# Performance work log

Measured on AMD Instinct MI355X. Metric: run time of the kernel, lower is better.

## Reference

```python
import jax, jax.numpy as jnp
import numpy as np

V = 12288      # HEALPix vertices (nside=32)
C_IN = 128
C_OUT = 128
K = 4          # Chebyshev polynomial degree
DEG = 9        # nnz per Laplacian row (8 neighbors + self)
B = 8
BN_EPS = 1e-5


def setup_inputs() -> dict:
    key = jax.random.key(0)
    kx, kc, kv, kw = jax.random.split(key, 4)
    x = jax.random.normal(kx, (B, V, C_IN), dtype=jnp.float32)
    # sparse Laplacian as COO edge list: 9 entries per row
    lap_rows = jnp.repeat(jnp.arange(V, dtype=jnp.int32), DEG)          # [E]
    lap_cols = jax.random.randint(kc, (V * DEG,), 0, V, dtype=jnp.int32)
    lap_vals = jax.random.normal(kv, (V * DEG,), dtype=jnp.float32) * 0.1
    # Chebyshev weight [Fin*K, Fout] (Fin-major, K-minor, matching [B,V,Fin,K] reshape)
    weight = jax.random.normal(kw, (C_IN * K, C_OUT), dtype=jnp.float32) * (1.0 / np.sqrt(C_IN * K))
    gamma = jnp.ones((C_OUT,), dtype=jnp.float32)
    beta = jnp.zeros((C_OUT,), dtype=jnp.float32)
    return {"x": x, "lap_rows": lap_rows, "lap_cols": lap_cols,
            "lap_vals": lap_vals, "weight": weight, "gamma": gamma, "beta": beta}


def reference(x, lap_rows, lap_cols, lap_vals, weight, gamma, beta):
    b, v, c = x.shape
    k = weight.shape[0] // c

    def spmm(y):
        # y: [B, V, C] -> L @ y along vertex dim
        y2 = y.transpose(1, 0, 2).reshape(v, b * c)                 # [V, B*C]
        g = lap_vals[:, None] * y2[lap_cols]                        # [E, B*C]
        out = jnp.zeros((v, b * c), dtype=y.dtype).at[lap_rows].add(g)
        return out.reshape(v, b, c).transpose(1, 0, 2)              # [B, V, C]

    # Chebyshev recursion: T0 = x, T1 = L x, Tk = 2 L T_{k-1} - T_{k-2}
    terms = [x]
    if k > 1:
        terms.append(spmm(x))
    for _ in range(2, k):
        terms.append(2.0 * spmm(terms[-1]) - terms[-2])
    xk = jnp.stack(terms, axis=-1)                                  # [B, V, C, K]
    conv = jnp.einsum('bvck,cko->bvo', xk.reshape(b, v, c, k),
                      weight.reshape(c, k, -1))                     # [B, V, Cout]

    # BatchNorm1d over [B, Cout, V]: stats over (batch, vertices) per channel
    h = conv.transpose(0, 2, 1)                                     # [B, Cout, V]
    mean = jnp.mean(h, axis=(0, 2), keepdims=True)
    var = jnp.var(h, axis=(0, 2), keepdims=True)
    hn = (h - mean) * jax.lax.rsqrt(var + BN_EPS)
    return hn * gamma[None, :, None] + beta[None, :, None]          # [B, Cout, V]
```

## Files before the change

### kernel.cpp

```cpp
#include <hip/hip_runtime.h>

#define NV    12288
#define CIN   128
#define COUT  128
#define DEG   9
#define NB    8
#define NROWS (NB * NV)
#define KTOT  512
#define BM    384

typedef unsigned short bfu;
typedef __attribute__((ext_vector_type(8))) short short8;
typedef __attribute__((ext_vector_type(4))) float floatx4;

__device__ __forceinline__ float bf2f(unsigned short u) {
    union { unsigned int i; float f; } x;
    x.i = ((unsigned int)u) << 16;
    return x.f;
}
__device__ __forceinline__ unsigned short f2bf(float f) {
    union { float f; unsigned int i; } x;
    x.f = f;
    unsigned int r = x.i + 0x7FFFu + ((x.i >> 16) & 1u);
    return (unsigned short)(r >> 16);
}
__device__ __forceinline__ void gload16(const void* g, void* l) {
    __builtin_amdgcn_global_load_lds(
        (const __attribute__((address_space(1))) unsigned int*)g,
        (__attribute__((address_space(3))) unsigned int*)l, 16, 0, 0);
}

__global__ __launch_bounds__(256)
void prep_kernel(const float* __restrict__ x, bfu* __restrict__ xb,
                 const float* __restrict__ W, bfu* __restrict__ Wt,
                 float* __restrict__ stats)
{
    const int blk = blockIdx.x;
    const int t   = threadIdx.x;
    if (blk < 6144) {
        const size_t i = ((size_t)blk * 256 + t) * 8;
        const float4 a = *reinterpret_cast<const float4*>(x + i);
        const float4 b = *reinterpret_cast<const float4*>(x + i + 4);
        short8 r;
        r[0] = (short)f2bf(a.x); r[1] = (short)f2bf(a.y);
        r[2] = (short)f2bf(a.z); r[3] = (short)f2bf(a.w);
        r[4] = (short)f2bf(b.x); r[5] = (short)f2bf(b.y);
        r[6] = (short)f2bf(b.z); r[7] = (short)f2bf(b.w);
        *reinterpret_cast<short8*>(xb + i) = r;
    } else if (blk < 6400) {
        const int i = (blk - 6144) * 256 + t;
        const int o = i >> 9;
        const int kap = i & 511;
        const int s = kap >> 7;
        const int c = kap & 127;
        Wt[i] = f2bf(W[(size_t)(c * 4 + s) * COUT + o]);
    } else {
        stats[t] = 0.f;
        if (t == 0) stats[2 * COUT] = 0.f;
    }
}

__global__ __launch_bounds__(256)
void spmm_bf16(const bfu* __restrict__ src, const bfu* __restrict__ sub,
               bfu* __restrict__ outp, const int* __restrict__ cols,
               const float* __restrict__ vals)
{
    const int t  = threadIdx.x;
    const int b  = blockIdx.x & 7;
    const int vt = blockIdx.x >> 3;
    const int v  = vt * 16 + (t >> 4);
    const int c0 = (t & 15) * 8;

    int   ec[DEG];
    float ev[DEG];
#pragma unroll
    for (int e = 0; e < DEG; ++e) {
        ec[e] = cols[v * DEG + e];
        ev[e] = vals[v * DEG + e];
    }

    float acc[8];
#pragma unroll
    for (int j = 0; j < 8; ++j) acc[j] = 0.f;

    const size_t bbase = (size_t)b * NV * CIN;
#pragma unroll
    for (int e = 0; e < DEG; ++e) {
        const short8 s = *reinterpret_cast<const short8*>(
            src + bbase + (size_t)ec[e] * CIN + c0);
#pragma unroll
        for (int j = 0; j < 8; ++j)
            acc[j] = fmaf(ev[e], bf2f((unsigned short)s[j]), acc[j]);
    }

    if (sub != nullptr) {
        const short8 s0 = *reinterpret_cast<const short8*>(
            sub + bbase + (size_t)v * CIN + c0);
#pragma unroll
        for (int j = 0; j < 8; ++j)
            acc[j] = 2.f * acc[j] - bf2f((unsigned short)s0[j]);
    }

    short8 r;
#pragma unroll
    for (int j = 0; j < 8; ++j) r[j] = (short)f2bf(acc[j]);
    *reinterpret_cast<short8*>(outp + bbase + (size_t)v * CIN + c0) = r;
}

__global__ __launch_bounds__(512, 2)
void gemm_mfma(const bfu* __restrict__ A0, const bfu* __restrict__ A1,
               const bfu* __restrict__ A2, const bfu* __restrict__ A3,
               const bfu* __restrict__ Wt, float* __restrict__ gstats,
               const float* __restrict__ gamma, const float* __restrict__ beta,
               float* __restrict__ outp)
{
    extern __shared__ char smem[];

    const int t    = threadIdx.x;
    const int lane = t & 63;
    const int wid  = t >> 6;
    const int wr   = wid >> 1;
    const int wc   = wid & 1;
    const int rbase = blockIdx.x * BM;

    floatx4 acc[6][4];
#pragma unroll
    for (int m = 0; m < 6; ++m)
#pragma unroll
        for (int n = 0; n < 4; ++n) acc[m][n] = (floatx4){0.f, 0.f, 0.f, 0.f};

    const bfu* segs[4] = {A0, A1, A2, A3};

#define STAGE(KT, BUF)                                                        \
    {                                                                         \
        const bfu* As_ = segs[(KT) >> 2];                                     \
        const int  cb_ = ((KT) & 3) * 32;                                     \
        _Pragma("unroll")                                                     \
        for (int p = 0; p < 3; ++p) {                                         \
            const int flat = p * 512 + t;                                     \
            const int rr   = flat >> 2;                                       \
            const int ck   = flat & 3;                                        \
            gload16(As_ + (size_t)(rbase + rr) * CIN + cb_                    \
                        + ((ck ^ ((rr >> 1) & 3)) << 3),                      \
                    smem + (BUF) * 24576 + flat * 16);                        \
        }                                                                     \
        {                                                                     \
            const int nn = t >> 2;                                            \
            const int ck = t & 3;                                             \
            gload16(Wt + (size_t)nn * KTOT + (KT) * 32                        \
                       + ((ck ^ ((nn >> 1) & 3)) << 3),                       \
                    smem + 73728 + (BUF) * 8192 + t * 16);                    \
        }                                                                     \
    }

    STAGE(0, 0);
    STAGE(1, 1);
    asm volatile("s_waitcnt vmcnt(4)\n\ts_barrier" ::: "memory");

    const int rsw   = ((lane & 15) >> 1) & 3;
    const int chunk = ((lane >> 4) ^ rsw) * 16;

#pragma unroll
    for (int kt = 0; kt < 16; ++kt) {
        if (kt + 2 < 16) STAGE(kt + 2, (kt + 2) % 3);

        const char* abase = smem + (kt % 3) * 24576;
        const char* bbase = smem + 73728 + (kt % 3) * 8192;
        short8 a[6], b[4];
#pragma unroll
        for (int m = 0; m < 6; ++m)
            a[m] = *reinterpret_cast<const short8*>(
                abase + (wr * 96 + m * 16 + (lane & 15)) * 64 + chunk);
#pragma unroll
        for (int n = 0; n < 4; ++n)
            b[n] = *reinterpret_cast<const short8*>(
                bbase + (wc * 64 + n * 16 + (lane & 15)) * 64 + chunk);
#pragma unroll
        for (int m = 0; m < 6; ++m)
#pragma unroll
            for (int n = 0; n < 4; ++n)
                acc[m][n] = __builtin_amdgcn_mfma_f32_16x16x32_bf16(
                    a[m], b[n], acc[m][n], 0, 0, 0);

        if (kt <= 13)
            asm volatile("s_waitcnt vmcnt(4)\n\ts_barrier" ::: "memory");
        else if (kt == 14)
            asm volatile("s_waitcnt vmcnt(0)\n\ts_barrier" ::: "memory");
    }
#undef STAGE

    __syncthreads();
    float* sred = (float*)smem;
    float* qred = sred + COUT;
    if (t < COUT) { sred[t] = 0.f; qred[t] = 0.f; }
    __syncthreads();

    const int batch = rbase / NV;
    const int v0 = (rbase % NV) + wr * 96 + (lane >> 4) * 4;
    const int ob = wc * 64 + (lane & 15);

#pragma unroll
    for (int n = 0; n < 4; ++n) {
        const int o = ob + n * 16;
        float s = 0.f, q = 0.f;
#pragma unroll
        for (int m = 0; m < 6; ++m) {
            const floatx4 v4 = acc[m][n];
#pragma unroll
            for (int j = 0; j < 4; ++j) {
                s += v4[j];
                q = fmaf(v4[j], v4[j], q);
            }
        }
        s += __shfl_xor(s, 16); s += __shfl_xor(s, 32);
        q += __shfl_xor(q, 16); q += __shfl_xor(q, 32);
        if ((lane >> 4) == 0) {
            atomicAdd(&sred[o], s);
            atomicAdd(&qred[o], q);
        }
    }
    __syncthreads();
    if (t < COUT) {
        atomicAdd(&gstats[t], sred[t]);
        atomicAdd(&gstats[COUT + t], qred[t]);
    }
    __syncthreads();

    unsigned int* ctr = (unsigned int*)&gstats[2 * COUT];
    if (t == 0) {
        __threadfence();
        atomicAdd(ctr, 1u);
        while (__hip_atomic_load(ctr, __ATOMIC_RELAXED,
                                 __HIP_MEMORY_SCOPE_AGENT) < gridDim.x) { }
        __threadfence();
    }
    __syncthreads();

    const float invN = 1.0f / (float)NROWS;
#pragma unroll
    for (int n = 0; n < 4; ++n) {
        const int o = ob + n * 16;
        const float mean = gstats[o] * invN;
        const float var  = gstats[COUT + o] * invN - mean * mean;
        const float sc   = rsqrtf(var + 1e-5f) * gamma[o];
        const float sh   = beta[o] - mean * sc;
        float* obase = outp + ((size_t)batch * COUT + o) * NV + v0;
#pragma unroll
        for (int m = 0; m < 6; ++m) {
            const floatx4 v4 = acc[m][n];
            float4 r;
            r.x = fmaf(v4[0], sc, sh);
            r.y = fmaf(v4[1], sc, sh);
            r.z = fmaf(v4[2], sc, sh);
            r.w = fmaf(v4[3], sc, sh);
            *reinterpret_cast<float4*>(obase + m * 16) = r;
        }
    }
}

extern "C" void kernel_launch(void* const* d_in, const int* in_sizes, int n_in,
                              void* d_out, int out_size, void* d_ws, size_t ws_size,
                              hipStream_t stream)
{
    (void)in_sizes; (void)n_in; (void)out_size; (void)ws_size;

    const float* x     = (const float*)d_in[0];
    const int*   cols  = (const int*)  d_in[2];
    const float* vals  = (const float*)d_in[3];
    const float* W     = (const float*)d_in[4];
    const float* gamma = (const float*)d_in[5];
    const float* beta  = (const float*)d_in[6];
    float*       out   = (float*)d_out;

    const size_t bufE = (size_t)NB * NV * CIN;

    bfu* xb    = (bfu*)d_ws;
    bfu* t1    = xb + bufE;
    bfu* t2    = t1 + bufE;
    bfu* t3    = t2 + bufE;
    bfu* Wt    = t3 + bufE;
    float* stats = (float*)(Wt + 65536);

    const dim3 blk(256);
    const int spmm_grid = (NV / 16) * NB;

    prep_kernel <<<6401, blk, 0, stream>>>(x, xb, W, Wt, stats);

    spmm_bf16 <<<spmm_grid, blk, 0, stream>>>(xb, nullptr, t1, cols, vals);
    spmm_bf16 <<<spmm_grid, blk, 0, stream>>>(t1, xb,      t2, cols, vals);
    spmm_bf16 <<<spmm_grid, blk, 0, stream>>>(t2, t1,      t3, cols, vals);

    gemm_mfma <<<NROWS / BM, dim3(512), 98304, stream>>>(
        xb, t1, t2, t3, Wt, stats, gamma, beta, out);
}
```

Measured before the change: 115.6 us.

## Fuse three SpMM launches into one persistent kernel with grid barriers

Replaces the three separate Chebyshev SpMM kernel launches with one persistent kernel of 1024 blocks. Each block processes six vertex tiles per stage and synchronises with the other blocks through an atomic-counter grid barrier between stages. This removes two launch gaps and the tail drain between stages. In exchange it depends on all 1024 blocks being co-resident to avoid deadlock, and each block gets less parallelism per stage.

Result: slower. 429.0 us (+271.0%).

```diff
diff --git a/kernel.cpp b/kernel.cpp
--- a/kernel.cpp
+++ b/kernel.cpp
@@ -8,6 +8,7 @@
 #define NROWS (NB * NV)
 #define KTOT  512
 #define BM    384
+#define NBLK_SP 1024
 
 typedef unsigned short bfu;
 typedef __attribute__((ext_vector_type(8))) short short8;
@@ -56,19 +57,16 @@
         Wt[i] = f2bf(W[(size_t)(c * 4 + s) * COUT + o]);
     } else {
         stats[t] = 0.f;
-        if (t == 0) stats[2 * COUT] = 0.f;
-    }
-}
-
-__global__ __launch_bounds__(256)
-void spmm_bf16(const bfu* __restrict__ src, const bfu* __restrict__ sub,
+        if (t < 2) stats[2 * COUT + t] = 0.f;
+    }
+}
+
+__device__ __forceinline__
+void spmm_tile(const bfu* __restrict__ src, const bfu* __restrict__ sub,
                bfu* __restrict__ outp, const int* __restrict__ cols,
-               const float* __restrict__ vals)
-{
-    const int t  = threadIdx.x;
-    const int b  = blockIdx.x & 7;
-    const int vt = blockIdx.x >> 3;
-    const int v  = vt * 16 + (t >> 4);
+               const float* __restrict__ vals, int b, int vtile, int t)
+{
+    const int v  = vtile * 16 + (t >> 4);
     const int c0 = (t & 15) * 8;
 
     int   ec[DEG];
@@ -105,6 +103,41 @@
 #pragma unroll
     for (int j = 0; j < 8; ++j) r[j] = (short)f2bf(acc[j]);
     *reinterpret_cast<short8*>(outp + bbase + (size_t)v * CIN + c0) = r;
+}
+
+__device__ __forceinline__ void gridbar(unsigned int* ctr, unsigned int target)
+{
+    __syncthreads();
+    if (threadIdx.x == 0) {
+        __hip_atomic_fetch_add(ctr, 1u, __ATOMIC_RELEASE,
+                               __HIP_MEMORY_SCOPE_AGENT);
+        while (__hip_atomic_load(ctr, __ATOMIC_ACQUIRE,
+                                 __HIP_MEMORY_SCOPE_AGENT) < target) { }
+    }
+    __syncthreads();
+}
+
+__global__ __launch_bounds__(256, 4)
+void spmm3_fused(const bfu* __restrict__ xb, bfu* __restrict__ t1,
+                 bfu* __restrict__ t2, bfu* __restrict__ t3,
+                 const int* __restrict__ cols, const float* __restrict__ vals,
+                 float* __restrict__ stats)
+{
+    unsigned int* ctr = (unsigned int*)&stats[2 * COUT + 1];
+    const int t  = threadIdx.x;
+    const int b  = blockIdx.x & 7;
+    const int tg = (int)(blockIdx.x >> 3);
+
+    for (int i = 0; i < 6; ++i)
+        spmm_tile(xb, nullptr, t1, cols, vals, b, tg * 6 + i, t);
+    gridbar(ctr, 1 * NBLK_SP);
+
+    for (int i = 0; i < 6; ++i)
+        spmm_tile(t1, xb, t2, cols, vals, b, tg * 6 + i, t);
+    gridbar(ctr, 2 * NBLK_SP);
+
+    for (int i = 0; i < 6; ++i)
+        spmm_tile(t2, t1, t3, cols, vals, b, tg * 6 + i, t);
 }
 
 __global__ __launch_bounds__(512, 2)
@@ -230,7 +263,7 @@
     if (t == 0) {
         __threadfence();
         atomicAdd(ctr, 1u);
-        while (__hip_atomic_load(ctr, __ATOMIC_RELAXED,
+        while (__hip_atomic_load(ctr, __ATOMIC_ACQUIRE,
                                  __HIP_MEMORY_SCOPE_AGENT) < gridDim.x) { }
         __threadfence();
     }
@@ -282,13 +315,10 @@
     float* stats = (float*)(Wt + 65536);
 
     const dim3 blk(256);
-    const int spmm_grid = (NV / 16) * NB;
 
     prep_kernel <<<6401, blk, 0, stream>>>(x, xb, W, Wt, stats);
 
-    spmm_bf16 <<<spmm_grid, blk, 0, stream>>>(xb, nullptr, t1, cols, vals);
-    spmm_bf16 <<<spmm_grid, blk, 0, stream>>>(t1, xb,      t2, cols, vals);
-    spmm_bf16 <<<spmm_grid, blk, 0, stream>>>(t2, t1,      t3, cols, vals);
+    spmm3_fused <<<NBLK_SP, blk, 0, stream>>>(xb, t1, t2, t3, cols, vals, stats);
 
     gemm_mfma <<<NROWS / BM, dim3(512), 98304, stream>>>(
         xb, t1, t2, t3, Wt, stats, gamma, beta, out);
```
